# Performance work log

Measured on AMD Instinct MI355X. Metric: run time of the kernel, lower is better.

## Reference

```python
import jax, jax.numpy as jnp
import numpy as np

B, N, K = 4, 8192, 64
COS_EPS = 1e-8


def _conv_bn_relu(x, W, b, g, bt):
    # 1x1 conv over channels + eval-mode BatchNorm (running mean 0, var 1) + ReLU
    x = jnp.einsum('bcn,oc->bon', x, W) + b[None, :, None]
    x = x * g[None, :, None] + bt[None, :, None]
    return jax.nn.relu(x)


def _forward(imageneighbors, knnpoints, points, feature_2d3d,
             sift_W, sift_b, sift_g, sift_bt,
             c2_W1, c2_b1, c2_g1, c2_bt1, c2_W2, c2_b2, c2_g2, c2_bt2,
             lin1_W, lin1_b,
             c3_W1, c3_b1, c3_g1, c3_bt1, c3_W2, c3_b2, c3_g2, c3_bt2,
             pn2_W, pn2_b, pn2_g, pn2_bt,
             fw1, fw2, fw3):
    b, _, n = points.shape
    # forward: imageneighbors.permute(0,1,3,2)  [b,3,n,K] -> [b,3,K,n]
    img = jnp.transpose(imageneighbors, (0, 1, 3, 2))
    # geometric_similarity: both neighbor sets as [b,3,n,K]
    real_nk = jnp.transpose(knnpoints, (0, 1, 3, 2))   # [b,3,n,K]
    img_nk = imageneighbors                            # [b,3,n,K]
    # knn_distance: per-point pairwise sq-dists between real and image neighbors
    r2 = jnp.sum(real_nk ** 2, axis=1)                 # [b,n,K]
    i2 = jnp.sum(img_nk ** 2, axis=1)                  # [b,n,K]
    cross = jnp.einsum('bcnk,bcnl->bnkl', real_nk, img_nk)
    d = r2[..., :, None] + i2[..., None, :] - 2.0 * cross  # [b,n,K,K]
    min_dist = jnp.min(d, axis=(2, 3))                 # [b,n] == distance[:,:,0]

    furthest_image_repre = img.reshape(b, -1, n)       # [b,192,n]
    furthest_real_repre = knnpoints.reshape(b, -1, n)  # [b,192,n]

    def shallow(repre):
        x = jnp.concatenate([points, repre], axis=1)   # [b,195,n]
        x = _conv_bn_relu(x, sift_W, sift_b, sift_g, sift_bt)  # PointSIFT-> 128
        x = _conv_bn_relu(x, c2_W1, c2_b1, c2_g1, c2_bt1)      # 128->64
        x = _conv_bn_relu(x, c2_W2, c2_b2, c2_g2, c2_bt2)      # 64->64
        return x

    shallowrealfeat = shallow(furthest_real_repre)
    shallowimagefeat = shallow(furthest_image_repre)

    sr1 = jnp.einsum('bcn,oc->bon', shallowrealfeat, lin1_W) + lin1_b[None, :, None]
    si1 = jnp.einsum('bcn,oc->bon', shallowimagefeat, lin1_W) + lin1_b[None, :, None]
    num = jnp.sum(sr1 * si1, axis=1)
    den = jnp.maximum(jnp.linalg.norm(sr1, axis=1) * jnp.linalg.norm(si1, axis=1), COS_EPS)
    cos_sim = num / den                                # [b,n]

    geo = jnp.exp(-(1.0 / fw1[0]) * min_dist) + fw2[0]
    shallow_similarity = cos_sim * geo                 # [b,n]

    f2d3d = shallow_similarity[:, None, :] * feature_2d3d      # [b,64,n]
    fused = jnp.concatenate([shallowrealfeat, f2d3d], axis=1)  # [b,128,n]
    fused = _conv_bn_relu(fused, c3_W1, c3_b1, c3_g1, c3_bt1)  # 128->64
    fused = _conv_bn_relu(fused, c3_W2, c3_b2, c3_g2, c3_bt2)  # 64->64

    deep_in = jnp.concatenate([points, fused], axis=1)         # [b,67,n]
    deeprealfeat = _conv_bn_relu(deep_in, pn2_W, pn2_b, pn2_g, pn2_bt)  # PN2 emb -> 128

    deep_similarity = jnp.ones_like(shallow_similarity) * fw3[0]
    return (shallow_similarity, deep_similarity, shallowrealfeat, deeprealfeat)


def setup_inputs() -> dict:
    key = jax.random.key(0)
    ks = jax.random.split(key, 24)

    def nrm(k, shape, s=1.0):
        return jax.random.normal(k, shape, dtype=jnp.float32) * s

    def w(k, out_c, in_c):
        return nrm(k, (out_c, in_c), 1.0 / np.sqrt(in_c))

    points = nrm(ks[0], (B, 3, N))
    knnpoints = jnp.transpose(points[:, :, None, :], (0, 1, 2, 3)) + nrm(ks[1], (B, 3, K, N), 0.1)
    imageneighbors = points[:, :, :, None] + nrm(ks[2], (B, 3, N, K), 0.1)
    feature_2d3d = nrm(ks[3], (B, 64, N))

    inp = {
        'imageneighbors': imageneighbors,
        'knnpoints': knnpoints,
        'points': points,
        'feature_2d3d': feature_2d3d,
        'sift_W': w(ks[4], 128, 195), 'sift_b': jnp.zeros(128), 'sift_g': jnp.ones(128), 'sift_bt': jnp.zeros(128),
        'c2_W1': w(ks[5], 64, 128), 'c2_b1': jnp.zeros(64), 'c2_g1': jnp.ones(64), 'c2_bt1': jnp.zeros(64),
        'c2_W2': w(ks[6], 64, 64), 'c2_b2': jnp.zeros(64), 'c2_g2': jnp.ones(64), 'c2_bt2': jnp.zeros(64),
        'lin1_W': w(ks[7], 64, 64), 'lin1_b': jnp.zeros(64),
        'c3_W1': w(ks[8], 64, 128), 'c3_b1': jnp.zeros(64), 'c3_g1': jnp.ones(64), 'c3_bt1': jnp.zeros(64),
        'c3_W2': w(ks[9], 64, 64), 'c3_b2': jnp.zeros(64), 'c3_g2': jnp.ones(64), 'c3_bt2': jnp.zeros(64),
        'pn2_W': w(ks[10], 128, 67), 'pn2_b': jnp.zeros(128), 'pn2_g': jnp.ones(128), 'pn2_bt': jnp.zeros(128),
        'fw1': jnp.full((1,), 0.25, dtype=jnp.float32),
        'fw2': jnp.zeros((1,), dtype=jnp.float32),
        'fw3': jnp.ones((1,), dtype=jnp.float32),
    }
    return inp


def reference(imageneighbors, knnpoints, points, feature_2d3d,
              sift_W, sift_b, sift_g, sift_bt,
              c2_W1, c2_b1, c2_g1, c2_bt1, c2_W2, c2_b2, c2_g2, c2_bt2,
              lin1_W, lin1_b,
              c3_W1, c3_b1, c3_g1, c3_bt1, c3_W2, c3_b2, c3_g2, c3_bt2,
              pn2_W, pn2_b, pn2_g, pn2_bt,
              fw1, fw2, fw3):
    return _forward(imageneighbors, knnpoints, points, feature_2d3d,
                    sift_W, sift_b, sift_g, sift_bt,
                    c2_W1, c2_b1, c2_g1, c2_bt1, c2_W2, c2_b2, c2_g2, c2_bt2,
                    lin1_W, lin1_b,
                    c3_W1, c3_b1, c3_g1, c3_bt1, c3_W2, c3_b2, c3_g2, c3_bt2,
                    pn2_W, pn2_b, pn2_g, pn2_bt,
                    fw1, fw2, fw3)
```

## Files before the change

kernel.cpp:

```cpp
#include <hip/hip_runtime.h>
#include <hip/hip_bf16.h>
#include <math.h>

typedef __attribute__((ext_vector_type(8))) short short8;
typedef __attribute__((ext_vector_type(4))) float f32x4;
typedef __attribute__((ext_vector_type(16))) float f32x16;
typedef unsigned short ushort_t;

#define N_PTS 8192

#define WP1   0
#define WP2A  28672
#define WP2B  36864
#define WLIN  40960
#define WC3A  45056
#define WC3B  53248
#define WPN   57344
#define FBF   34816
#define FB_L1 0
#define FB_2A 128
#define FB_2B 192
#define FB_LIN 256
#define FB_3A 320
#define FB_3B 384
#define FB_PN 448

#define OUT_SIM  0
#define OUT_DSIM 32768
#define OUT_SHAL 65536
#define OUT_DEEP 2162688

#define ST1 232
#define ST2 168
#define ST3 104
#define S_X1  0
#define S_X2  7424
#define S_X3A 12800
#define S_X3B 16128
#define S_X4  0
#define S_F2  1664

__device__ __forceinline__ ushort_t f2bf(float x) {
    __hip_bfloat16 hv = __float2bfloat16(x);
    return *reinterpret_cast<ushort_t*>(&hv);
}
__device__ __forceinline__ float bf2f(ushort_t h) {
    return __uint_as_float(((unsigned)h) << 16);
}

__global__ __launch_bounds__(256)
void prep_all(const float* __restrict__ sW, const float* __restrict__ sb,
              const float* __restrict__ sg, const float* __restrict__ sbt,
              const float* __restrict__ aW, const float* __restrict__ ab,
              const float* __restrict__ ag, const float* __restrict__ abt,
              const float* __restrict__ bW, const float* __restrict__ bb_,
              const float* __restrict__ bg, const float* __restrict__ bbt,
              const float* __restrict__ lW, const float* __restrict__ lb,
              const float* __restrict__ cW, const float* __restrict__ cb,
              const float* __restrict__ cg, const float* __restrict__ cbt,
              const float* __restrict__ dW, const float* __restrict__ db,
              const float* __restrict__ dg, const float* __restrict__ dbt,
              const float* __restrict__ pW, const float* __restrict__ pb,
              const float* __restrict__ pg, const float* __restrict__ pbt,
              ushort_t* __restrict__ wsp) {
    int g = blockIdx.x * 256 + threadIdx.x;
    if (g >= 9280) return;
    if (g >= 8704) {
        int idx = g - 8704;
        const float *B, *G, *BT; int m, has_bn;
        if (idx < 128)      { B=sb;  G=sg; BT=sbt; m=idx;       has_bn=1; }
        else if (idx < 192) { B=ab;  G=ag; BT=abt; m=idx-128;   has_bn=1; }
        else if (idx < 256) { B=bb_; G=bg; BT=bbt; m=idx-192;   has_bn=1; }
        else if (idx < 320) { B=lb;  G=lb; BT=lb;  m=idx-256;   has_bn=0; }
        else if (idx < 384) { B=cb;  G=cg; BT=cbt; m=idx-320;   has_bn=1; }
        else if (idx < 448) { B=db;  G=dg; BT=dbt; m=idx-384;   has_bn=1; }
        else                { B=pb;  G=pg; BT=pbt; m=idx-448;   has_bn=1; }
        ((float*)wsp)[FBF + idx] = has_bn ? fmaf(G[m], B[m], BT[m]) : B[m];
        return;
    }
    const float *W, *G;
    int in_c, KS, mode, has_bn, off;
    if (g < 3584)      {           W=sW; G=sg; in_c=195; KS=7; mode=1; has_bn=1; off=WP1;  }
    else if (g < 4608) { g -= 3584; W=aW; G=ag; in_c=128; KS=4; mode=0; has_bn=1; off=WP2A; }
    else if (g < 5120) { g -= 4608; W=bW; G=bg; in_c=64;  KS=2; mode=0; has_bn=1; off=WP2B; }
    else if (g < 5632) { g -= 5120; W=lW; G=lW; in_c=64;  KS=2; mode=0; has_bn=0; off=WLIN; }
    else if (g < 6656) { g -= 5632; W=cW; G=cg; in_c=128; KS=4; mode=0; has_bn=1; off=WC3A; }
    else if (g < 7168) { g -= 6656; W=dW; G=dg; in_c=64;  KS=2; mode=0; has_bn=1; off=WC3B; }
    else               { g -= 7168; W=pW; G=pg; in_c=67;  KS=3; mode=2; has_bn=1; off=WPN;  }

    int lane = g & 63, u = g >> 6, ks = u % KS, mt = u / KS;
    int m  = mt * 16 + (lane & 15);
    int k0 = ks * 32 + ((lane >> 4) << 3);
    float scale = has_bn ? G[m] : 1.0f;
    ushort_t o[8];
    #pragma unroll
    for (int i = 0; i < 8; ++i) {
        int k = k0 + i; float v = 0.0f;
        if (mode == 1) {
            if (k < 192)      v = W[m * 195 + 3 + k] * scale;
            else if (k < 195) v = W[m * 195 + (k - 192)] * scale;
        } else if (mode == 2) {
            if (k < 64)       v = W[m * 67 + 3 + k] * scale;
            else if (k < 67)  v = W[m * 67 + (k - 64)] * scale;
        } else {
            if (k < in_c)     v = W[m * in_c + k] * scale;
        }
        o[i] = f2bf(v);
    }
    ushort4 lo, hi;
    lo.x = o[0]; lo.y = o[1]; lo.z = o[2]; lo.w = o[3];
    hi.x = o[4]; hi.y = o[5]; hi.z = o[6]; hi.w = o[7];
    int t = (((mt * KS + ks) * 64) + lane) * 8 + off;
    *(ushort4*)(wsp + t)     = lo;
    *(ushort4*)(wsp + t + 4) = hi;
}

template<int KS, int NTS>
__device__ __forceinline__ void mfma_tiles(const short8* __restrict__ WP,
                                           const float* __restrict__ fb,
                                           int mt, int nt0,
                                           const ushort_t* __restrict__ Xin, int sin,
                                           int lane, f32x4 acc[NTS]) {
    float4 b4 = *(const float4*)(fb + mt * 16 + ((lane >> 4) << 2));
    #pragma unroll
    for (int t = 0; t < NTS; ++t) acc[t] = (f32x4){b4.x, b4.y, b4.z, b4.w};
    #pragma unroll
    for (int ks = 0; ks < KS; ++ks) {
        short8 a = WP[(mt * KS + ks) * 64 + lane];
        #pragma unroll
        for (int t = 0; t < NTS; ++t) {
            const short8 bv = *(const short8*)(Xin + ((lane & 15) + (nt0 + t) * 16) * sin
                                               + ks * 32 + ((lane >> 4) << 3));
            acc[t] = __builtin_amdgcn_mfma_f32_16x16x32_bf16(a, bv, acc[t], 0, 0, 0);
        }
    }
}

template<int NTS>
__device__ __forceinline__ void epi_relu_lds(const f32x4 acc[NTS], int mt, int nt0,
                                             int h, int p, ushort_t* Xout, int sout) {
    int ch0 = mt * 16 + h * 4;
    #pragma unroll
    for (int t = 0; t < NTS; ++t) {
        int pt = p + (nt0 + t) * 16;
        ushort4 u;
        u.x = f2bf(fmaxf(acc[t].x, 0.f)); u.y = f2bf(fmaxf(acc[t].y, 0.f));
        u.z = f2bf(fmaxf(acc[t].z, 0.f)); u.w = f2bf(fmaxf(acc[t].w, 0.f));
        *(ushort4*)(Xout + pt * sout + ch0) = u;
    }
}

__device__ __forceinline__ float fold16(const f32x16 a) {
    float t0 = fminf(fminf(a[0], a[1]), a[2]);
    float t1 = fminf(fminf(a[3], a[4]), a[5]);
    float t2 = fminf(fminf(a[6], a[7]), a[8]);
    float t3 = fminf(fminf(a[9], a[10]), a[11]);
    float t4 = fminf(fminf(a[12], a[13]), a[14]);
    float s0 = fminf(fminf(t0, t1), t2);
    float s1 = fminf(fminf(t3, t4), a[15]);
    return fminf(s0, s1);
}

__device__ __forceinline__ void dist_point(const ushort_t* __restrict__ X1base,
                                           int pt, int lane, float* __restrict__ DMIN) {
    const short8 zero8 = {0, 0, 0, 0, 0, 0, 0, 0};
    const int m32 = lane & 31;
    const int h2  = lane >> 5;
    const ushort_t* rrow = X1base + pt * ST1;
    const ushort_t* irow = X1base + (16 + pt) * ST1;
    float px = bf2f(rrow[192]), py = bf2f(rrow[193]), pz = bf2f(rrow[194]);
    short8 af[2], bfr[2];
    #pragma unroll
    for (int c = 0; c < 2; ++c) {
        int k = c * 32 + m32;
        float rx = bf2f(rrow[k]) - px;
        float ry = bf2f(rrow[64 + k]) - py;
        float rz = bf2f(rrow[128 + k]) - pz;
        float r2 = fmaf(rx, rx, fmaf(ry, ry, rz * rz));
        short8 t = zero8;
        t[0] = (short)f2bf(-2.0f * rx); t[1] = (short)f2bf(-2.0f * ry);
        t[2] = (short)f2bf(-2.0f * rz); t[3] = (short)f2bf(r2);
        t[4] = (short)0x3F80;
        af[c] = h2 ? zero8 : t;
        float fx = bf2f(irow[k]) - px;
        float fy = bf2f(irow[64 + k]) - py;
        float fz = bf2f(irow[128 + k]) - pz;
        float i2 = fmaf(fx, fx, fmaf(fy, fy, fz * fz));
        short8 s = zero8;
        s[0] = (short)f2bf(fx); s[1] = (short)f2bf(fy); s[2] = (short)f2bf(fz);
        s[3] = (short)0x3F80;   s[4] = (short)f2bf(i2);
        bfr[c] = h2 ? zero8 : s;
    }
    float dmin = 3.0e38f;
    #pragma unroll
    for (int kc = 0; kc < 2; ++kc) {
        #pragma unroll
        for (int lc = 0; lc < 2; ++lc) {
            f32x16 acc = {0.f,0.f,0.f,0.f,0.f,0.f,0.f,0.f,
                          0.f,0.f,0.f,0.f,0.f,0.f,0.f,0.f};
            acc = __builtin_amdgcn_mfma_f32_32x32x16_bf16(af[kc], bfr[lc], acc, 0, 0, 0);
            dmin = fminf(dmin, fold16(acc));
        }
    }
    #pragma unroll
    for (int off = 32; off > 0; off >>= 1)
        dmin = fminf(dmin, __shfl_xor(dmin, off, 64));
    if (lane == 0) DMIN[pt] = dmin;
}

__global__ __launch_bounds__(512, 8)
void fused_all(const float* __restrict__ img,
               const float* __restrict__ knn,
               const float* __restrict__ pts,
               const float* __restrict__ f2d,
               const float* __restrict__ fw1p, const float* __restrict__ fw2p,
               const float* __restrict__ fw3p,
               const ushort_t* __restrict__ wsp, float* __restrict__ out)
{
    __shared__ ushort_t SMEM[19456];
    __shared__ float DMIN[16];
    __shared__ float RBUF[3][4][16];

    const int tid  = threadIdx.x;
    const int wid  = __builtin_amdgcn_readfirstlane(tid >> 6);
    const int lane = tid & 63;
    const int p16  = lane & 15;
    const int h    = lane >> 4;
    const int b    = blockIdx.x >> 9;
    const int n0   = (blockIdx.x & 511) << 4;

    const int mt64 = wid & 3;
    const int nt1  = wid >> 2;

    const float* fbias = (const float*)wsp + FBF;
    f32x4 a2[2], a1[1];
    float fpre[4] = {0.f, 0.f, 0.f, 0.f};

    for (int e = tid; e < 32 * 29; e += 512) {
        int r = e / 29, c = 195 + e % 29;
        SMEM[S_X1 + r * ST1 + c] = 0;
    }
    {
        int pt = tid & 15, g = tid >> 4;
        #pragma unroll
        for (int jp = 0; jp < 3; ++jp) {
            int ck = g * 6 + jp * 2;
            int c = ck >> 6, k = ck & 63;
            const float* base = knn + ((size_t)(b * 3 + c) * 64 + k) * N_PTS + n0 + pt;
            ushort2 u;
            u.x = f2bf(base[0]);
            u.y = f2bf(base[(size_t)N_PTS]);
            *(ushort2*)(SMEM + S_X1 + pt * ST1 + ck) = u;
        }
    }
    {
        int pt = tid >> 5, q = tid & 31;
        #pragma unroll
        for (int c = 0; c < 3; ++c) {
            float2 v = *(const float2*)(img + (((size_t)(b * 3 + c)) * N_PTS + n0 + pt) * 64 + q * 2);
            ushort2 u;
            u.x = f2bf(v.x); u.y = f2bf(v.y);
            *(ushort2*)(SMEM + S_X1 + (16 + pt) * ST1 + c * 64 + q * 2) = u;
        }
    }
    if (tid < 96) {
        int c = tid >> 5, r = tid & 31;
        SMEM[S_X1 + r * ST1 + 192 + c] = f2bf(pts[((size_t)(b * 3 + c)) * N_PTS + n0 + (r & 15)]);
    }
    __syncthreads();

    mfma_tiles<7, 2>((const short8*)(wsp + WP1), fbias + FB_L1, wid, 0,
                     SMEM + S_X1, ST1, lane, a2);
    epi_relu_lds<2>(a2, wid, 0, h, p16, SMEM + S_X2, ST2);
    __syncthreads();

    mfma_tiles<4, 1>((const short8*)(wsp + WP2A), fbias + FB_2A, mt64, nt1,
                     SMEM + S_X2, ST2, lane, a1);
    epi_relu_lds<1>(a1, mt64, nt1, h, p16, SMEM + S_X3A, ST3);
    dist_point(SMEM + S_X1, wid * 2, lane, DMIN);
    __syncthreads();

    mfma_tiles<2, 1>((const short8*)(wsp + WP2B), fbias + FB_2B, mt64, nt1,
                     SMEM + S_X3A, ST3, lane, a1);
    {
        int ch0 = mt64 * 16 + h * 4;
        int row = p16 + nt1 * 16;
        float v0 = fmaxf(a1[0].x, 0.f), v1 = fmaxf(a1[0].y, 0.f);
        float v2 = fmaxf(a1[0].z, 0.f), v3 = fmaxf(a1[0].w, 0.f);
        ushort4 u;
        u.x = f2bf(v0); u.y = f2bf(v1); u.z = f2bf(v2); u.w = f2bf(v3);
        *(ushort4*)(SMEM + S_X3B + row * ST3 + ch0) = u;
        if (nt1 == 0) {
            size_t base = OUT_SHAL + ((size_t)(b * 64 + ch0)) * N_PTS + n0 + p16;
            out[base]             = v0;
            out[base + N_PTS]     = v1;
            out[base + 2 * N_PTS] = v2;
            out[base + 3 * N_PTS] = v3;
        }
    }
    dist_point(SMEM + S_X1, wid * 2 + 1, lane, DMIN);
    __syncthreads();

    if (wid < 4) {
        f32x4 sv[2];
        mfma_tiles<2, 2>((const short8*)(wsp + WLIN), fbias + FB_LIN, wid, 0,
                         SMEM + S_X3B, ST3, lane, sv);
        float pn = sv[0].x * sv[1].x + sv[0].y * sv[1].y + sv[0].z * sv[1].z + sv[0].w * sv[1].w;
        float pr = sv[0].x * sv[0].x + sv[0].y * sv[0].y + sv[0].z * sv[0].z + sv[0].w * sv[0].w;
        float pi = sv[1].x * sv[1].x + sv[1].y * sv[1].y + sv[1].z * sv[1].z + sv[1].w * sv[1].w;
        pn += __shfl_xor(pn, 16, 64); pn += __shfl_xor(pn, 32, 64);
        pr += __shfl_xor(pr, 16, 64); pr += __shfl_xor(pr, 32, 64);
        pi += __shfl_xor(pi, 16, 64); pi += __shfl_xor(pi, 32, 64);
        if (lane < 16) {
            RBUF[0][wid][p16] = pn;
            RBUF[1][wid][p16] = pr;
            RBUF[2][wid][p16] = pi;
        }
    } else {
        int t256 = tid - 256;
        int pt = t256 & 15, cg = t256 >> 4;
        #pragma unroll
        for (int r = 0; r < 4; ++r)
            fpre[r] = f2d[((size_t)(b * 64 + cg * 4 + r)) * N_PTS + n0 + pt];
        if (t256 < 48) {
            int c = t256 >> 4, r = t256 & 15;
            SMEM[S_X4 + r * ST3 + 64 + c] = f2bf(pts[((size_t)(b * 3 + c)) * N_PTS + n0 + r]);
        }
        for (int e = t256; e < 16 * 29; e += 256) {
            int r = e / 29, c = 67 + e % 29;
            SMEM[S_X4 + r * ST3 + c] = 0;
        }
    }
    __syncthreads();

    if (wid >= 4) {
        int t256 = tid - 256;
        int pt = t256 & 15, cg = t256 >> 4;
        float num = 0.f, rr = 0.f, ii = 0.f;
        #pragma unroll
        for (int m = 0; m < 4; ++m) {
            num += RBUF[0][m][pt];
            rr  += RBUF[1][m][pt];
            ii  += RBUF[2][m][pt];
        }
        float den = fmaxf(sqrtf(rr) * sqrtf(ii), 1e-8f);
        float geo = expf(-(1.0f / fw1p[0]) * DMIN[pt]) + fw2p[0];
        float sim = (num / den) * geo;
        ushort4 u;
        u.x = f2bf(sim * fpre[0]); u.y = f2bf(sim * fpre[1]);
        u.z = f2bf(sim * fpre[2]); u.w = f2bf(sim * fpre[3]);
        *(ushort4*)(SMEM + S_F2 + pt * ST3 + cg * 4) = u;
        if (cg == 0) {
            out[OUT_SIM  + (size_t)b * N_PTS + n0 + pt] = sim;
            out[OUT_DSIM + (size_t)b * N_PTS + n0 + pt] = fw3p[0];
        }
    }
    __syncthreads();

    if (wid < 4) {
        const short8* W = (const short8*)(wsp + WC3A);
        float4 b4 = *(const float4*)(fbias + FB_3A + wid * 16 + (h << 2));
        f32x4 a = (f32x4){b4.x, b4.y, b4.z, b4.w};
        int row = p16 * ST3 + (h << 3);
        #pragma unroll
        for (int ks = 0; ks < 4; ++ks) {
            short8 aw = W[(wid * 4 + ks) * 64 + lane];
            const ushort_t* src = (ks < 2)
                ? (SMEM + S_X3B + row + ks * 32)
                : (SMEM + S_F2  + row + (ks - 2) * 32);
            a = __builtin_amdgcn_mfma_f32_16x16x32_bf16(aw, *(const short8*)src, a, 0, 0, 0);
        }
        a1[0] = a;
        epi_relu_lds<1>(a1, wid, 0, h, p16, SMEM + S_X3A, ST3);
    }
    __syncthreads();

    if (wid < 4) {
        mfma_tiles<2, 1>((const short8*)(wsp + WC3B), fbias + FB_3B, wid, 0,
                         SMEM + S_X3A, ST3, lane, a1);
        epi_relu_lds<1>(a1, wid, 0, h, p16, SMEM + S_X4, ST3);
    }
    __syncthreads();

    mfma_tiles<3, 1>((const short8*)(wsp + WPN), fbias + FB_PN, wid, 0,
                     SMEM + S_X4, ST3, lane, a1);
    {
        int ch0 = wid * 16 + h * 4;
        size_t base = OUT_DEEP + ((size_t)(b * 128 + ch0)) * N_PTS + n0 + p16;
        out[base]             = fmaxf(a1[0].x, 0.f);
        out[base + N_PTS]     = fmaxf(a1[0].y, 0.f);
        out[base + 2 * N_PTS] = fmaxf(a1[0].z, 0.f);
        out[base + 3 * N_PTS] = fmaxf(a1[0].w, 0.f);
    }
}

extern "C" void kernel_launch(void* const* d_in, const int* in_sizes, int n_in,
                              void* d_out, int out_size, void* d_ws, size_t ws_size,
                              hipStream_t stream) {
    const float* img    = (const float*)d_in[0];
    const float* knn    = (const float*)d_in[1];
    const float* pts    = (const float*)d_in[2];
    const float* f2d    = (const float*)d_in[3];
    const float* sift_W = (const float*)d_in[4];
    const float* sift_b = (const float*)d_in[5];
    const float* sift_g = (const float*)d_in[6];
    const float* sift_bt= (const float*)d_in[7];
    const float* c2_W1  = (const float*)d_in[8];
    const float* c2_b1  = (const float*)d_in[9];
    const float* c2_g1  = (const float*)d_in[10];
    const float* c2_bt1 = (const float*)d_in[11];
    const float* c2_W2  = (const float*)d_in[12];
    const float* c2_b2  = (const float*)d_in[13];
    const float* c2_g2  = (const float*)d_in[14];
    const float* c2_bt2 = (const float*)d_in[15];
    const float* lin1_W = (const float*)d_in[16];
    const float* lin1_b = (const float*)d_in[17];
    const float* c3_W1  = (const float*)d_in[18];
    const float* c3_b1  = (const float*)d_in[19];
    const float* c3_g1  = (const float*)d_in[20];
    const float* c3_bt1 = (const float*)d_in[21];
    const float* c3_W2  = (const float*)d_in[22];
    const float* c3_b2  = (const float*)d_in[23];
    const float* c3_g2  = (const float*)d_in[24];
    const float* c3_bt2 = (const float*)d_in[25];
    const float* pn2_W  = (const float*)d_in[26];
    const float* pn2_b  = (const float*)d_in[27];
    const float* pn2_g  = (const float*)d_in[28];
    const float* pn2_bt = (const float*)d_in[29];
    const float* fw1    = (const float*)d_in[30];
    const float* fw2    = (const float*)d_in[31];
    const float* fw3    = (const float*)d_in[32];

    ushort_t* wsp = (ushort_t*)d_ws;
    float* out = (float*)d_out;

    prep_all<<<37, 256, 0, stream>>>(
        sift_W, sift_b, sift_g, sift_bt,
        c2_W1, c2_b1, c2_g1, c2_bt1,
        c2_W2, c2_b2, c2_g2, c2_bt2,
        lin1_W, lin1_b,
        c3_W1, c3_b1, c3_g1, c3_bt1,
        c3_W2, c3_b2, c3_g2, c3_bt2,
        pn2_W, pn2_b, pn2_g, pn2_bt,
        wsp);

    fused_all<<<2048, 512, 0, stream>>>(img, knn, pts, f2d, fw1, fw2, fw3, wsp, out);
}
```

Baseline: 42.07 us.

## Halve points per block to 8 with 256-thread blocks and 4096-block grid

Each block now handles 8 points instead of 16, using 4 waves instead of 8, and the grid doubles to 4096 blocks. Real and image rows are packed into one 16-row MFMA tile, and a lane shuffle pairs the real and image lin1 outputs for the cosine similarity. Shared memory per block is halved, which should allow more blocks per CU and more latency hiding. In exchange, per-block weight loads double across the grid, and half the MFMA N-dimension lanes are discarded on output stores.

```diff
diff --git a/kernel.cpp b/kernel.cpp
--- a/kernel.cpp
+++ b/kernel.cpp
@@ -34,9 +34,9 @@
 #define ST2 168
 #define ST3 104
 #define S_X1  0
-#define S_X2  7424
-#define S_X3A 12800
-#define S_X3B 16128
+#define S_X2  3712
+#define S_X3A 6400
+#define S_X3B 8064
 #define S_X4  0
 #define S_F2  1664
 
@@ -167,7 +167,7 @@
     const int m32 = lane & 31;
     const int h2  = lane >> 5;
     const ushort_t* rrow = X1base + pt * ST1;
-    const ushort_t* irow = X1base + (16 + pt) * ST1;
+    const ushort_t* irow = X1base + (8 + pt) * ST1;
     float px = bf2f(rrow[192]), py = bf2f(rrow[193]), pz = bf2f(rrow[194]);
     short8 af[2], bfr[2];
     #pragma unroll
@@ -208,7 +208,7 @@
     if (lane == 0) DMIN[pt] = dmin;
 }
 
-__global__ __launch_bounds__(512, 8)
+__global__ __launch_bounds__(256, 8)
 void fused_all(const float* __restrict__ img,
                const float* __restrict__ knn,
                const float* __restrict__ pts,
@@ -217,31 +217,28 @@
                const float* __restrict__ fw3p,
                const ushort_t* __restrict__ wsp, float* __restrict__ out)
 {
-    __shared__ ushort_t SMEM[19456];
-    __shared__ float DMIN[16];
-    __shared__ float RBUF[3][4][16];
+    __shared__ ushort_t SMEM[9728];
+    __shared__ float DMIN[8];
+    __shared__ float RBUF[3][4][8];
 
     const int tid  = threadIdx.x;
     const int wid  = __builtin_amdgcn_readfirstlane(tid >> 6);
     const int lane = tid & 63;
     const int p16  = lane & 15;
     const int h    = lane >> 4;
-    const int b    = blockIdx.x >> 9;
-    const int n0   = (blockIdx.x & 511) << 4;
-
-    const int mt64 = wid & 3;
-    const int nt1  = wid >> 2;
+    const int b    = blockIdx.x >> 10;
+    const int n0   = (blockIdx.x & 1023) << 3;
 
     const float* fbias = (const float*)wsp + FBF;
-    f32x4 a2[2], a1[1];
-    float fpre[4] = {0.f, 0.f, 0.f, 0.f};
-
-    for (int e = tid; e < 32 * 29; e += 512) {
+    f32x4 a1[1];
+    float fpre[2] = {0.f, 0.f};
+
+    for (int e = tid; e < 16 * 29; e += 256) {
         int r = e / 29, c = 195 + e % 29;
         SMEM[S_X1 + r * ST1 + c] = 0;
     }
     {
-        int pt = tid & 15, g = tid >> 4;
+        int pt = tid & 7, g = tid >> 3;
         #pragma unroll
         for (int jp = 0; jp < 3; ++jp) {
             int ck = g * 6 + jp * 2;
@@ -260,37 +257,40 @@
             float2 v = *(const float2*)(img + (((size_t)(b * 3 + c)) * N_PTS + n0 + pt) * 64 + q * 2);
             ushort2 u;
             u.x = f2bf(v.x); u.y = f2bf(v.y);
-            *(ushort2*)(SMEM + S_X1 + (16 + pt) * ST1 + c * 64 + q * 2) = u;
-        }
-    }
-    if (tid < 96) {
-        int c = tid >> 5, r = tid & 31;
-        SMEM[S_X1 + r * ST1 + 192 + c] = f2bf(pts[((size_t)(b * 3 + c)) * N_PTS + n0 + (r & 15)]);
-    }
-    __syncthreads();
-
-    mfma_tiles<7, 2>((const short8*)(wsp + WP1), fbias + FB_L1, wid, 0,
-                     SMEM + S_X1, ST1, lane, a2);
-    epi_relu_lds<2>(a2, wid, 0, h, p16, SMEM + S_X2, ST2);
-    __syncthreads();
-
-    mfma_tiles<4, 1>((const short8*)(wsp + WP2A), fbias + FB_2A, mt64, nt1,
+            *(ushort2*)(SMEM + S_X1 + (8 + pt) * ST1 + c * 64 + q * 2) = u;
+        }
+    }
+    if (tid < 48) {
+        int c = tid >> 4, r = tid & 15;
+        SMEM[S_X1 + r * ST1 + 192 + c] = f2bf(pts[((size_t)(b * 3 + c)) * N_PTS + n0 + (r & 7)]);
+    }
+    __syncthreads();
+
+    #pragma unroll
+    for (int s = 0; s < 2; ++s) {
+        int mt = wid * 2 + s;
+        mfma_tiles<7, 1>((const short8*)(wsp + WP1), fbias + FB_L1, mt, 0,
+                         SMEM + S_X1, ST1, lane, a1);
+        epi_relu_lds<1>(a1, mt, 0, h, p16, SMEM + S_X2, ST2);
+    }
+    __syncthreads();
+
+    mfma_tiles<4, 1>((const short8*)(wsp + WP2A), fbias + FB_2A, wid, 0,
                      SMEM + S_X2, ST2, lane, a1);
-    epi_relu_lds<1>(a1, mt64, nt1, h, p16, SMEM + S_X3A, ST3);
+    epi_relu_lds<1>(a1, wid, 0, h, p16, SMEM + S_X3A, ST3);
     dist_point(SMEM + S_X1, wid * 2, lane, DMIN);
     __syncthreads();
 
-    mfma_tiles<2, 1>((const short8*)(wsp + WP2B), fbias + FB_2B, mt64, nt1,
+    mfma_tiles<2, 1>((const short8*)(wsp + WP2B), fbias + FB_2B, wid, 0,
                      SMEM + S_X3A, ST3, lane, a1);
     {
-        int ch0 = mt64 * 16 + h * 4;
-        int row = p16 + nt1 * 16;
+        int ch0 = wid * 16 + h * 4;
         float v0 = fmaxf(a1[0].x, 0.f), v1 = fmaxf(a1[0].y, 0.f);
         float v2 = fmaxf(a1[0].z, 0.f), v3 = fmaxf(a1[0].w, 0.f);
         ushort4 u;
         u.x = f2bf(v0); u.y = f2bf(v1); u.z = f2bf(v2); u.w = f2bf(v3);
-        *(ushort4*)(SMEM + S_X3B + row * ST3 + ch0) = u;
-        if (nt1 == 0) {
+        *(ushort4*)(SMEM + S_X3B + p16 * ST3 + ch0) = u;
+        if (p16 < 8) {
             size_t base = OUT_SHAL + ((size_t)(b * 64 + ch0)) * N_PTS + n0 + p16;
             out[base]             = v0;
             out[base + N_PTS]     = v1;
@@ -301,41 +301,46 @@
     dist_point(SMEM + S_X1, wid * 2 + 1, lane, DMIN);
     __syncthreads();
 
-    if (wid < 4) {
-        f32x4 sv[2];
-        mfma_tiles<2, 2>((const short8*)(wsp + WLIN), fbias + FB_LIN, wid, 0,
+    {
+        f32x4 sv[1];
+        mfma_tiles<2, 1>((const short8*)(wsp + WLIN), fbias + FB_LIN, wid, 0,
                          SMEM + S_X3B, ST3, lane, sv);
-        float pn = sv[0].x * sv[1].x + sv[0].y * sv[1].y + sv[0].z * sv[1].z + sv[0].w * sv[1].w;
+        int src = (lane & 48) | ((lane + 8) & 15);
+        f32x4 sw;
+        sw.x = __shfl(sv[0].x, src, 64);
+        sw.y = __shfl(sv[0].y, src, 64);
+        sw.z = __shfl(sv[0].z, src, 64);
+        sw.w = __shfl(sv[0].w, src, 64);
+        float pn = sv[0].x * sw.x + sv[0].y * sw.y + sv[0].z * sw.z + sv[0].w * sw.w;
         float pr = sv[0].x * sv[0].x + sv[0].y * sv[0].y + sv[0].z * sv[0].z + sv[0].w * sv[0].w;
-        float pi = sv[1].x * sv[1].x + sv[1].y * sv[1].y + sv[1].z * sv[1].z + sv[1].w * sv[1].w;
+        float pi = sw.x * sw.x + sw.y * sw.y + sw.z * sw.z + sw.w * sw.w;
         pn += __shfl_xor(pn, 16, 64); pn += __shfl_xor(pn, 32, 64);
         pr += __shfl_xor(pr, 16, 64); pr += __shfl_xor(pr, 32, 64);
         pi += __shfl_xor(pi, 16, 64); pi += __shfl_xor(pi, 32, 64);
-        if (lane < 16) {
-            RBUF[0][wid][p16] = pn;
-            RBUF[1][wid][p16] = pr;
-            RBUF[2][wid][p16] = pi;
-        }
-    } else {
-        int t256 = tid - 256;
-        int pt = t256 & 15, cg = t256 >> 4;
-        #pragma unroll
-        for (int r = 0; r < 4; ++r)
-            fpre[r] = f2d[((size_t)(b * 64 + cg * 4 + r)) * N_PTS + n0 + pt];
-        if (t256 < 48) {
-            int c = t256 >> 4, r = t256 & 15;
+        if (lane < 8) {
+            RBUF[0][wid][lane] = pn;
+            RBUF[1][wid][lane] = pr;
+            RBUF[2][wid][lane] = pi;
+        }
+    }
+    {
+        int pt = tid & 7, cg = tid >> 3;
+        const float* fb2 = f2d + ((size_t)(b * 64 + cg * 2)) * N_PTS + n0 + pt;
+        fpre[0] = fb2[0];
+        fpre[1] = fb2[(size_t)N_PTS];
+        if (tid < 24) {
+            int c = tid >> 3, r = tid & 7;
             SMEM[S_X4 + r * ST3 + 64 + c] = f2bf(pts[((size_t)(b * 3 + c)) * N_PTS + n0 + r]);
         }
-        for (int e = t256; e < 16 * 29; e += 256) {
+        for (int e = tid; e < 8 * 29; e += 256) {
             int r = e / 29, c = 67 + e % 29;
             SMEM[S_X4 + r * ST3 + c] = 0;
         }
     }
     __syncthreads();
 
-    if (wid >= 4) {
-        int t256 = tid - 256;
-        int pt = t256 & 15, cg = t256 >> 4;
+    {
+        int pt = tid & 7, cg = tid >> 3;
         float num = 0.f, rr = 0.f, ii = 0.f;
         #pragma unroll
         for (int m = 0; m < 4; ++m) {
@@ -346,10 +351,10 @@
         float den = fmaxf(sqrtf(rr) * sqrtf(ii), 1e-8f);
         float geo = expf(-(1.0f / fw1p[0]) * DMIN[pt]) + fw2p[0];
         float sim = (num / den) * geo;
-        ushort4 u;
-        u.x = f2bf(sim * fpre[0]); u.y = f2bf(sim * fpre[1]);
-        u.z = f2bf(sim * fpre[2]); u.w = f2bf(sim * fpre[3]);
-        *(ushort4*)(SMEM + S_F2 + pt * ST3 + cg * 4) = u;
+        ushort2 u;
+        u.x = f2bf(sim * fpre[0]);
+        u.y = f2bf(sim * fpre[1]);
+        *(ushort2*)(SMEM + S_F2 + pt * ST3 + cg * 2) = u;
         if (cg == 0) {
             out[OUT_SIM  + (size_t)b * N_PTS + n0 + pt] = sim;
             out[OUT_DSIM + (size_t)b * N_PTS + n0 + pt] = fw3p[0];
@@ -357,7 +362,7 @@
     }
     __syncthreads();
 
-    if (wid < 4) {
+    {
         const short8* W = (const short8*)(wsp + WC3A);
         float4 b4 = *(const float4*)(fbias + FB_3A + wid * 16 + (h << 2));
         f32x4 a = (f32x4){b4.x, b4.y, b4.z, b4.w};
@@ -375,22 +380,24 @@
     }
     __syncthreads();
 
-    if (wid < 4) {
-        mfma_tiles<2, 1>((const short8*)(wsp + WC3B), fbias + FB_3B, wid, 0,
-                         SMEM + S_X3A, ST3, lane, a1);
-        epi_relu_lds<1>(a1, wid, 0, h, p16, SMEM + S_X4, ST3);
-    }
-    __syncthreads();
-
-    mfma_tiles<3, 1>((const short8*)(wsp + WPN), fbias + FB_PN, wid, 0,
-                     SMEM + S_X4, ST3, lane, a1);
-    {
-        int ch0 = wid * 16 + h * 4;
-        size_t base = OUT_DEEP + ((size_t)(b * 128 + ch0)) * N_PTS + n0 + p16;
-        out[base]             = fmaxf(a1[0].x, 0.f);
-        out[base + N_PTS]     = fmaxf(a1[0].y, 0.f);
-        out[base + 2 * N_PTS] = fmaxf(a1[0].z, 0.f);
-        out[base + 3 * N_PTS] = fmaxf(a1[0].w, 0.f);
+    mfma_tiles<2, 1>((const short8*)(wsp + WC3B), fbias + FB_3B, wid, 0,
+                     SMEM + S_X3A, ST3, lane, a1);
+    epi_relu_lds<1>(a1, wid, 0, h, p16, SMEM + S_X4, ST3);
+    __syncthreads();
+
+    #pragma unroll
+    for (int s = 0; s < 2; ++s) {
+        int mt = wid * 2 + s;
+        mfma_tiles<3, 1>((const short8*)(wsp + WPN), fbias + FB_PN, mt, 0,
+                         SMEM + S_X4, ST3, lane, a1);
+        if (p16 < 8) {
+            int ch0 = mt * 16 + h * 4;
+            size_t base = OUT_DEEP + ((size_t)(b * 128 + ch0)) * N_PTS + n0 + p16;
+            out[base]             = fmaxf(a1[0].x, 0.f);
+            out[base + N_PTS]     = fmaxf(a1[0].y, 0.f);
+            out[base + 2 * N_PTS] = fmaxf(a1[0].z, 0.f);
+            out[base + 3 * N_PTS] = fmaxf(a1[0].w, 0.f);
+        }
     }
 }
 
@@ -444,5 +451,5 @@
         pn2_W, pn2_b, pn2_g, pn2_bt,
         wsp);
 
-    fused_all<<<2048, 512, 0, stream>>>(img, knn, pts, f2d, fw1, fw2, fw3, wsp, out);
-}
+    fused_all<<<4096, 256, 0, stream>>>(img, knn, pts, f2d, fw1, fw2, fw3, wsp, out);
+}
```

Result: slower. 58.73 us (+39.6%).
